# Kernel optimization log

Measured on AMD Instinct MI355X. Metric: run time of the kernel, lower is better.

Reference implementation:

```python
import jax, jax.numpy as jnp
import numpy as np

NT = 16          # nt_states
TS = 48          # t_states
T = NT + TS      # total states
B, N = 4, 24     # batch, sentence length
HUGE = 1.0e9


def setup_inputs():
    key = jax.random.key(0)
    k1, k2, k3 = jax.random.split(key, 3)
    unary_scores = jax.nn.log_softmax(jax.random.normal(k1, (B, N, T), jnp.float32), axis=-1)
    rule = jax.random.normal(k2, (B, NT, N, T, T, 2), jnp.float32)
    rule_scores = jax.nn.log_softmax(rule.reshape(B, NT, N, -1), axis=-1).reshape(B, NT, N, T, T, 2)
    root_scores = jax.nn.log_softmax(jax.random.normal(k3, (B, NT), jnp.float32), axis=-1)
    return {"unary_scores": unary_scores, "rule_scores": rule_scores, "root_scores": root_scores}


def _lse(x, axes):
    return jax.nn.logsumexp(x, axis=axes)


def _inside(unary_scores, rule_scores, root_scores):
    Bv, Nv, Tt = unary_scores.shape
    nt = rule_scores.shape[1]
    dt = unary_scores.dtype
    R = jnp.moveaxis(rule_scores, 5, 0)            # (D, B, Tparent, H, TL, TR)

    # beta[b,l,r,t,h]: headed inside chart; betau[b,l,r,t]: head-summed chart
    beta = jnp.full((Bv, Nv + 1, Nv + 1, Tt, Nv), -HUGE, dt)
    betau = jnp.full((Bv, Nv + 1, Nv + 1, Tt), -HUGE, dt)

    # width-1 spans: only terminal states (word_span_slice = nt:T, nt_emission=False)
    ks = np.arange(Nv)
    st = np.arange(nt, Tt)
    beta = beta.at[:, ks[:, None], ks[:, None] + 1, st[None, :], ks[:, None]].set(0.0)
    betau = betau.at[:, ks[:, None], ks[:, None] + 1, st[None, :]].set(
        unary_scores[:, ks[:, None], st[None, :]])

    nts = np.arange(nt)
    for W in range(2, Nv + 1):
        L = Nv - W + 1
        ls = np.arange(L)
        rs = ls + W
        hidx = ls[:, None] + np.arange(W)          # (L, W) absolute head positions

        def width_body(beta, betau, R, unary_scores, W=W, ls=ls, rs=rs, hidx=hidx):
            def chartH(la, ra, s0, s1):            # (B, L, S, W)
                x = beta[:, la, ra, s0:s1, :]
                return jnp.take_along_axis(x, hidx[None, :, None, :], axis=3)

            def chartU(la, ra, s0, s1):            # (B, L, S)
                return betau[:, la, ra, s0:s1]

            def rwin(d, a0, a1, c0, c1):           # (B, L, nt, W, A, C)
                r = R[d][:, :, hidx, a0:a1, c0:c1]
                return jnp.transpose(r, (0, 2, 1, 3, 4, 5))

            def comb(xH, yU, xU, yH, z0, z1):
                # D=0: head from left child; D=1: head from right child.
                # logsumexp over TL, TR and both directions -> (B, L, nt, W)
                left = (jnp.transpose(xH, (0, 1, 3, 2))[:, :, None, :, :, None]
                        + yU[:, :, None, None, None, :] + z0)
                right = (xU[:, :, None, None, :, None]
                         + jnp.transpose(yH, (0, 1, 3, 2))[:, :, None, :, None, :] + z1)
                return jnp.logaddexp(_lse(left, (-2, -1)), _lse(right, (-2, -1)))

            c0, c1 = (nt, Tt) if W == 2 else (0, nt)
            # split at l+1: left child is a single terminal
            tmp = comb(chartH(ls, ls + 1, nt, Tt), chartU(ls + 1, rs, c0, c1),
                       chartU(ls, ls + 1, nt, Tt), chartH(ls + 1, rs, c0, c1),
                       rwin(0, nt, Tt, c0, c1), rwin(1, nt, Tt, c0, c1))
            if W >= 3:
                # split at r-1: right child is a single terminal
                tmp = jnp.logaddexp(tmp, comb(
                    chartH(ls, rs - 1, 0, nt), chartU(rs - 1, rs, nt, Tt),
                    chartU(ls, rs - 1, 0, nt), chartH(rs - 1, rs, nt, Tt),
                    rwin(0, 0, nt, nt, Tt), rwin(1, 0, nt, nt, Tt)))
            if W >= 4:
                # interior splits: both children are nonterminal spans
                z0 = rwin(0, 0, nt, 0, nt)
                z1 = rwin(1, 0, nt, 0, nt)
                for wl in range(2, W - 1):
                    s = ls + wl
                    tmp = jnp.logaddexp(tmp, comb(
                        chartH(ls, s, 0, nt), chartU(s, rs, 0, nt),
                        chartU(ls, s, 0, nt), chartH(s, rs, 0, nt), z0, z1))
            # add head-word emission under the parent NT; sum heads for betau
            uw = jnp.transpose(unary_scores[:, hidx, :nt], (0, 1, 3, 2))  # (B,L,nt,W)
            return tmp, _lse(tmp + uw, -1)

        tmp, tmpu = jax.checkpoint(width_body)(beta, betau, R, unary_scores)
        beta = beta.at[:, ls[:, None, None], rs[:, None, None],
                       nts[None, :, None], hidx[:, None, :]].set(tmp)
        betau = betau.at[:, ls[:, None], rs[:, None], nts[None, :]].set(tmpu)

    return jax.nn.logsumexp(betau[:, 0, Nv, :nt] + root_scores, axis=-1)  # log Z, (B,)


_inside_jit = jax.jit(_inside)


def reference(unary_scores, rule_scores, root_scores):
    return _inside_jit(unary_scores, rule_scores, root_scores)
```

## Files before the change

kernel.cpp:

```cpp
#include <hip/hip_runtime.h>
#include <cstddef>

#define Bv 4
#define Nv 24
#define NTv 16
#define Tv 64
#define NP 25
#define NEGF (-1e30f)

#define BETAA_OFF 0
#define BETAU_OFF 960000
#define RNT_OFF   1120000
#define T0_OFF    1906432
#define T1_OFF    2496256
#define T0L_OFF   3086080
#define T1R_OFF   3110656
#define D0_OFF    3135232
#define D1_OFF    3136768
#define EU_OFF    3138304
#define PROG_OFF  3142912
#define WS_NEED   3143040

__device__ __forceinline__ void publish(float* p, float v) {
  *p = v;
  (void)__hip_atomic_exchange(p, v, __ATOMIC_RELAXED, __HIP_MEMORY_SCOPE_AGENT);
}

__global__ void init_kernel(const float* __restrict__ unary, float* __restrict__ betau,
                            float* __restrict__ Eu, int* __restrict__ prog) {
  int t = blockIdx.x * blockDim.x + threadIdx.x;
  if (t < Bv * 32) prog[t] = 0;
  if (t >= Bv * Nv * 48) return;
  int i = t % 48, kk = (t / 48) % Nv, b = t / (48 * Nv);
  float u = unary[(size_t)(b * Nv + kk) * Tv + 16 + i];
  betau[((size_t)(b * NP + kk) * NP + (kk + 1)) * Tv + 16 + i] = u;
  Eu[(size_t)(b * Nv + kk) * 48 + i] = __expf(u);
}

__global__ __launch_bounds__(256) void prep_kernel(
    const float* __restrict__ rule, const float* __restrict__ Eu,
    float* __restrict__ RNT, float* __restrict__ T0, float* __restrict__ T1,
    float* __restrict__ T0L, float* __restrict__ T1R,
    float* __restrict__ D0, float* __restrict__ D1) {
  const int h = blockIdx.x, A = blockIdx.y, b = blockIdx.z;
  const int t = threadIdx.x;
  __shared__ float er0[64 * 65];
  __shared__ float er1[64 * 65];
  __shared__ float E[24 * 48];
  __shared__ float red[256];

  for (int i = t; i < 24 * 48; i += 256) E[i] = Eu[(size_t)b * (24 * 48) + i];
  const float* rb = rule + (size_t)((b * NTv + A) * Nv + h) * 8192;
#pragma unroll
  for (int i = 0; i < 8; ++i) {
    int lin = i * 1024 + t * 4;
    float4 v = *(const float4*)(rb + lin);
    int sL = lin >> 7, rem = (lin & 127) >> 1;
    er0[sL * 65 + rem] = __expf(v.x);
    er1[sL * 65 + rem] = __expf(v.y);
    er0[sL * 65 + rem + 1] = __expf(v.z);
    er1[sL * 65 + rem + 1] = __expf(v.w);
  }
  __syncthreads();
  {
    float* dst0 = RNT + (((size_t)(b * 2 + 0) * Nv + h) * NTv + A) * 256;
    float* dst1 = RNT + (((size_t)(b * 2 + 1) * Nv + h) * NTv + A) * 256;
    dst0[t] = er0[(t >> 4) * 65 + (t & 15)];
    dst1[t] = er1[(t >> 4) * 65 + (t & 15)];
  }
  for (int o = t; o < 384; o += 256) {
    int p = o >> 4, sL = o & 15;
    const float* Ep = E + p * 48;
    const float* r0 = er0 + sL * 65 + 16;
    float acc = 0.f;
#pragma unroll 8
    for (int j = 0; j < 48; ++j) acc += Ep[j] * r0[j];
    T0[(((size_t)(b * Nv + h) * Nv + p) * NTv + sL) * NTv + A] = acc;
  }
  for (int o = t; o < 384; o += 256) {
    int p = o >> 4, sR = o & 15;
    const float* Ep = E + p * 48;
    float acc = 0.f;
#pragma unroll 8
    for (int i = 0; i < 48; ++i) acc += Ep[i] * er1[(16 + i) * 65 + sR];
    T1[(((size_t)(b * Nv + h) * Nv + p) * NTv + sR) * NTv + A] = acc;
  }
  if (t < 16) {
    float acc = 0.f;
    for (int i = 0; i < 48; ++i) acc += er0[(16 + i) * 65 + t];
    T0L[((size_t)(b * Nv + h) * NTv + t) * NTv + A] = acc;
  } else if (t < 32) {
    int sL = t - 16;
    float acc = 0.f;
    for (int j = 0; j < 48; ++j) acc += er1[sL * 65 + 16 + j];
    T1R[((size_t)(b * Nv + h) * NTv + sL) * NTv + A] = acc;
  }
  float acc0 = 0.f, acc1 = 0.f;
  const int hp = (h + 1 < 24) ? h + 1 : 0, hm = (h >= 1) ? h - 1 : 0;
  for (int e = t; e < 2304; e += 256) {
    int i = e / 48, j = e % 48;
    float r0 = er0[(16 + i) * 65 + 16 + j];
    float r1 = er1[(16 + i) * 65 + 16 + j];
    acc0 += E[hp * 48 + j] * r0;
    acc1 += E[hm * 48 + i] * r1;
  }
  red[t] = acc0;
  __syncthreads();
  if (t < 64) {
    float s = red[t] + red[t + 64] + red[t + 128] + red[t + 192];
#pragma unroll
    for (int off = 32; off; off >>= 1) s += __shfl_xor(s, off, 64);
    if (t == 0 && h <= 22) D0[((size_t)b * Nv + h) * NTv + A] = s;
  }
  __syncthreads();
  red[t] = acc1;
  __syncthreads();
  if (t < 64) {
    float s = red[t] + red[t + 64] + red[t + 128] + red[t + 192];
#pragma unroll
    for (int off = 32; off; off >>= 1) s += __shfl_xor(s, off, 64);
    if (t == 0 && h >= 1) D1[((size_t)b * Nv + (h - 1)) * NTv + A] = s;
  }
}

__device__ __forceinline__ float max16(float v) {
  v = fmaxf(v, __shfl_xor(v, 8, 16));
  v = fmaxf(v, __shfl_xor(v, 4, 16));
  v = fmaxf(v, __shfl_xor(v, 2, 16));
  v = fmaxf(v, __shfl_xor(v, 1, 16));
  return v;
}

__device__ __forceinline__ void edge_dot(float v0, float v1, float v2, float v3,
                                         const float* Tb, float& sh, float& S) {
  float mx = fmaxf(fmaxf(v0, v1), fmaxf(v2, v3));
  mx = fmaxf(mx, __shfl_xor(mx, 1, 64));
  mx = fmaxf(mx, __shfl_xor(mx, 2, 64));
  float dot = __expf(v0 - mx) * Tb[0] + __expf(v1 - mx) * Tb[16] +
              __expf(v2 - mx) * Tb[32] + __expf(v3 - mx) * Tb[48];
  dot += __shfl_xor(dot, 1, 64);
  dot += __shfl_xor(dot, 2, 64);
  sh = mx;
  S = dot;
}

#define MAXI 21

__global__ __launch_bounds__(768) void width_all_kernel(
    const float* __restrict__ unary, float* __restrict__ betaA, float* __restrict__ betau,
    const float* __restrict__ RNT, const float* __restrict__ T0, const float* __restrict__ T1,
    const float* __restrict__ T0L, const float* __restrict__ T1R,
    const float* __restrict__ D0, const float* __restrict__ D1,
    const float* __restrict__ root, float* __restrict__ out, int* __restrict__ colFlag) {
  const int rr = blockIdx.x, b = blockIdx.y;
  const int r = rr + 2;
  const int tid = threadIdx.x;
  int* flagb = colFlag + b * 32;

  __shared__ float chartC[23][384];
  __shared__ float buC[23][16];
  __shared__ float U0[24 * 256], U1[24 * 256];
  __shared__ float sG0[24], sG1[24];
  __shared__ float pM[2 * 24 * 16], pS[2 * 24 * 16];
  __shared__ float sTmp[16 * 24];

  for (int i = 0; i <= r - 2; ++i) {
    const int l = r - 2 - i;
    const int W = r - l;

    if (W >= 3) {
      if (tid < W - 2) {
        const int m = l + 2 + tid;
        while (__hip_atomic_load(&flagb[m], __ATOMIC_RELAXED,
                                 __HIP_MEMORY_SCOPE_AGENT) < m - l - 1)
          __builtin_amdgcn_s_sleep(1);
      }
      __syncthreads();
    }

    const int g = tid >> 5;
    const int k = tid & 31;
    float U0r[8], U1r[8];
#pragma unroll
    for (int j = 0; j < 8; ++j) { U0r[j] = 0.f; U1r[j] = 0.f; }
    float G0 = NEGF, G1 = NEGF;

    if (g < W) {
      const int hcol = l + g;
      float av1[MAXI], av0[MAXI];
      int e1 = min(l + g, r - 2);
      int cnt1 = e1 - (l + 2) + 1; if (cnt1 < 0) cnt1 = 0;
      if (k < 16) {
        const size_t base = ((size_t)(b * NP + l) * NP + (l + 2)) * Tv + k;
#pragma unroll
        for (int ii = 0; ii < MAXI; ++ii)
          if (ii < cnt1) av1[ii] = betau[base + (size_t)ii * Tv];
      } else {
#pragma unroll
        for (int ii = 0; ii < MAXI; ++ii)
          if (ii < cnt1) av1[ii] = chartC[l + 2 + ii][hcol * 16 + (k - 16)];
      }
      int m0 = max(l + g + 1, l + 2), e0 = r - 2;
      int cnt0 = e0 - m0 + 1; if (cnt0 < 0) cnt0 = 0;
      if (k < 16) {
        const size_t base = ((size_t)(b * NP + l) * NP + m0) * 384 + (size_t)hcol * 16 + k;
#pragma unroll
        for (int ii = 0; ii < MAXI; ++ii)
          if (ii < cnt0) av0[ii] = betaA[base + (size_t)ii * 384];
      } else {
#pragma unroll
        for (int ii = 0; ii < MAXI; ++ii)
          if (ii < cnt0) av0[ii] = buC[m0 + ii][k - 16];
      }
      float mx1 = NEGF, mx0 = NEGF;
#pragma unroll
      for (int ii = 0; ii < MAXI; ++ii) {
        if (ii < cnt1) mx1 = fmaxf(mx1, av1[ii]);
        if (ii < cnt0) mx0 = fmaxf(mx0, av0[ii]);
      }
      float o1 = max16(mx1), o0 = max16(mx0);
      float t1 = __shfl_xor(o1, 16, 32), t0 = __shfl_xor(o0, 16, 32);
      G1 = o1 + t1;
      G0 = o0 + t0;
#pragma unroll
      for (int ii = 0; ii < MAXI; ++ii) {
        if (ii < cnt1) {
          float e = __expf(av1[ii] - o1);
          float eR = __shfl(e, 16 + (k & 15), 32);
#pragma unroll
          for (int j = 0; j < 8; ++j)
            U1r[j] += __shfl(e, 2 * j + (k >> 4), 32) * eR;
        }
        if (ii < cnt0) {
          float e = __expf(av0[ii] - o0);
          float eR = __shfl(e, 16 + (k & 15), 32);
#pragma unroll
          for (int j = 0; j < 8; ++j)
            U0r[j] += __shfl(e, 2 * j + (k >> 4), 32) * eR;
        }
      }
#pragma unroll
      for (int j = 0; j < 8; ++j) {
        U0[g * 256 + k + 32 * j] = U0r[j];
        U1[g * 256 + k + 32 * j] = U1r[j];
      }
      if (k == 0) { sG0[g] = G0; sG1[g] = G1; }
    }
    __syncthreads();

    {
      const int w = tid >> 6, lane = tid & 63;
      const int A = lane >> 2, q = lane & 3;
      for (int p = w; p < 2 * W; p += 12) {
        const int hh = p >> 1, d = p & 1;
        const int h = l + hh;
        const float* Urow = (d ? U1 : U0) + hh * 256 + 4 * q;
        const float* Rb = RNT + (((size_t)(b * 2 + d) * Nv + h) * NTv + A) * 256 + 4 * q;
        float a0 = 0.f, a1 = 0.f, a2 = 0.f, a3 = 0.f;
#pragma unroll
        for (int sL = 0; sL < 16; ++sL) {
          float4 u = *(const float4*)(Urow + sL * 16);
          float4 rv = *(const float4*)(Rb + sL * 16);
          a0 += u.x * rv.x; a1 += u.y * rv.y; a2 += u.z * rv.z; a3 += u.w * rv.w;
        }
        float acc = (a0 + a1) + (a2 + a3);
        acc += __shfl_xor(acc, 1, 64);
        acc += __shfl_xor(acc, 2, 64);
        float Mi = d ? sG1[hh] : sG0[hh];
        float sh2 = NEGF, S2 = 0.f, sh3 = NEGF, S3 = 0.f;
        if (W >= 3) {
          if (d == 0) {
            if (hh < W - 1) {
              const float* Tb = T0 + (((size_t)(b * Nv + h) * Nv + (r - 1)) * NTv + 4 * q) * NTv + A;
              float4 e4 = *(const float4*)(betaA +
                  ((size_t)(b * NP + l) * NP + (r - 1)) * 384 + (size_t)h * 16 + 4 * q);
              edge_dot(e4.x, e4.y, e4.z, e4.w, Tb, sh2, S2);
            }
            if (hh == 0) {
              const float* Tb = T0L + ((size_t)(b * Nv + l) * NTv + 4 * q) * NTv + A;
              const float* u4 = &buC[l + 1][4 * q];
              edge_dot(u4[0], u4[1], u4[2], u4[3], Tb, sh3, S3);
            }
          } else {
            if (hh >= 1) {
              const float* Tb = T1 + (((size_t)(b * Nv + h) * Nv + l) * NTv + 4 * q) * NTv + A;
              const float* e4 = &chartC[l + 1][h * 16 + 4 * q];
              edge_dot(e4[0], e4[1], e4[2], e4[3], Tb, sh2, S2);
            }
            if (hh == W - 1) {
              const float* Tb = T1R + ((size_t)(b * Nv + (r - 1)) * NTv + 4 * q) * NTv + A;
              float4 u4 = *(const float4*)(betau +
                  ((size_t)(b * NP + l) * NP + (r - 1)) * Tv + 4 * q);
              edge_dot(u4.x, u4.y, u4.z, u4.w, Tb, sh3, S3);
            }
          }
        } else {
          if (d == 0 && hh == 0) { sh2 = 0.f; S2 = D0[((size_t)b * Nv + l) * NTv + A]; }
          if (d == 1 && hh == 1) { sh2 = 0.f; S2 = D1[((size_t)b * Nv + l) * NTv + A]; }
        }
        float Mf = fmaxf(Mi, fmaxf(sh2, sh3));
        float Sf = acc * __expf(Mi - Mf) + S2 * __expf(sh2 - Mf) + S3 * __expf(sh3 - Mf);
        if (q == 0) {
          pM[(d * 24 + hh) * 16 + A] = Mf;
          pS[(d * 24 + hh) * 16 + A] = Sf;
        }
      }
    }
    __syncthreads();

    if (tid < 384) {
      int A2 = tid & 15, hh = tid >> 4;
      if (hh < W) {
        float M0 = pM[(0 * 24 + hh) * 16 + A2], S0 = pS[(0 * 24 + hh) * 16 + A2];
        float M1 = pM[(1 * 24 + hh) * 16 + A2], S1 = pS[(1 * 24 + hh) * 16 + A2];
        float nm = fmaxf(M0, M1);
        float s = S0 * __expf(M0 - nm) + S1 * __expf(M1 - nm);
        float val = nm + __logf(s);
        publish(&betaA[((size_t)(b * NP + l) * NP + r) * 384 + (l + hh) * 16 + A2], val);
        chartC[l][(l + hh) * 16 + A2] = val;
        sTmp[A2 * 24 + hh] = val + unary[(size_t)(b * Nv + (l + hh)) * Tv + A2];
      }
    }
    __syncthreads();
    if (tid < 16) {
      float mx = NEGF;
      for (int x = 0; x < W; ++x) mx = fmaxf(mx, sTmp[tid * 24 + x]);
      float s = 0.f;
      for (int x = 0; x < W; ++x) s += __expf(sTmp[tid * 24 + x] - mx);
      float val = mx + __logf(s);
      publish(&betau[((size_t)(b * NP + l) * NP + r) * Tv + tid], val);
      buC[l][tid] = val;
    }
    if (tid == 0) {
      asm volatile("s_waitcnt vmcnt(0)" ::: "memory");
      (void)__hip_atomic_exchange(&flagb[r], i + 1, __ATOMIC_RELAXED,
                                  __HIP_MEMORY_SCOPE_AGENT);
    }
  }

  if (rr == 22) {
    __syncthreads();
    if (tid == 0) {
      float vals[NTv];
      float mx = NEGF;
#pragma unroll
      for (int A = 0; A < NTv; ++A) {
        float v = buC[0][A] + root[b * NTv + A];
        vals[A] = v;
        mx = fmaxf(mx, v);
      }
      float s = 0.f;
#pragma unroll
      for (int A = 0; A < NTv; ++A) s += __expf(vals[A] - mx);
      out[b] = mx + __logf(s);
    }
  }
}

__global__ __launch_bounds__(768) void width_kernel_fb(
    const float* __restrict__ unary, const float* __restrict__ rule,
    float* __restrict__ betaA, float* __restrict__ betau, int W) {
  const int l = blockIdx.x, b = blockIdx.y;
  const int r = l + W;
  const int tid = threadIdx.x;
  const int sub = tid & 1;
  const int pid = tid >> 1;
  const int A = pid & 15;
  const int hh = pid >> 4;
  const int h = l + hh;
  const bool act = (hh < W);
  const int sA = tid & 15, sH = tid >> 4;

  __shared__ float sER0[48], sEL1[48];
  __shared__ float sCL0[16 * 24], sCR1[16 * 24];
  __shared__ float sMaxL0[24], sMaxR1[24];
  __shared__ float sShR0, sShL1;
  __shared__ float sTmp[16 * 24];

  float runM = NEGF, runS = 0.f;
  for (int m = l + 1; m < r; ++m) {
    const int wl = m - l, wr = r - m;
    if (tid < 64) {
      const int n = (wr == 1) ? 48 : 16, s0 = (wr == 1) ? 16 : 0;
      float v = (tid < n) ? betau[(size_t)((b * NP + m) * NP + r) * Tv + s0 + tid] : NEGF;
      float mx = v;
#pragma unroll
      for (int off = 32; off; off >>= 1) mx = fmaxf(mx, __shfl_xor(mx, off, 64));
      if (tid == 0) sShR0 = mx;
      if (tid < n) sER0[tid] = v - mx;
    } else if (tid < 128) {
      const int j = tid - 64;
      const int n = (wl == 1) ? 48 : 16, s0 = (wl == 1) ? 16 : 0;
      float v = (j < n) ? betau[(size_t)((b * NP + l) * NP + m) * Tv + s0 + j] : NEGF;
      float mx = v;
#pragma unroll
      for (int off = 32; off; off >>= 1) mx = fmaxf(mx, __shfl_xor(mx, off, 64));
      if (j == 0) sShL1 = mx;
      if (j < n) sEL1[j] = v - mx;
    }
    if (tid < 384) {
      if (wl > 1 && sH < wl) {
        float v = betaA[(size_t)((b * NP + l) * NP + m) * 384 + sA * Nv + (l + sH)];
        float mx = v;
#pragma unroll
        for (int off = 8; off; off >>= 1) mx = fmaxf(mx, __shfl_xor(mx, off, 16));
        if (sA == 0) sMaxL0[sH] = mx;
        sCL0[sA * Nv + sH] = v - mx;
      }
      if (wr > 1 && sH >= wl && sH < W) {
        float v = betaA[(size_t)((b * NP + m) * NP + r) * 384 + sA * Nv + (l + sH)];
        float mx = v;
#pragma unroll
        for (int off = 8; off; off >>= 1) mx = fmaxf(mx, __shfl_xor(mx, off, 16));
        if (sA == 0) sMaxR1[sH] = mx;
        sCR1[sA * Nv + sH] = v - mx;
      }
    }
    __syncthreads();
    if (act) {
      if (hh < wl && (wl > 1 || hh == 0)) {
        const int nL = (wl == 1) ? 48 : 16, sL0 = (wl == 1) ? 16 : 0;
        const int nR = (wr == 1) ? 48 : 16, sR0 = (wr == 1) ? 16 : 0;
        const float shift = ((wl == 1) ? 0.f : sMaxL0[hh]) + sShR0;
        float part = 0.f;
        const float* rb = rule + (size_t)(((b * NTv + A) * Nv + h) * Tv) * Tv * 2;
        for (int i = sub; i < nL; i += 2) {
          const float cl = (wl == 1) ? 0.f : sCL0[i * Nv + hh];
          const float* rp = rb + (size_t)(sL0 + i) * Tv * 2 + sR0 * 2;
#pragma unroll 8
          for (int j = 0; j < nR; ++j) part += __expf(cl + sER0[j] + rp[j * 2]);
        }
        float nm = fmaxf(runM, shift);
        runS = runS * __expf(runM - nm) + part * __expf(shift - nm);
        runM = nm;
      }
      if (hh >= wl && (wr > 1 || hh == W - 1)) {
        const int nL = (wl == 1) ? 48 : 16, sL0 = (wl == 1) ? 16 : 0;
        const int nR = (wr == 1) ? 48 : 16, sR0 = (wr == 1) ? 16 : 0;
        const float shift = sShL1 + ((wr == 1) ? 0.f : sMaxR1[hh]);
        float part = 0.f;
        const float* rb = rule + (size_t)(((b * NTv + A) * Nv + h) * Tv) * Tv * 2 + 1;
        for (int i = sub; i < nL; i += 2) {
          const float el = sEL1[i];
          const float* rp = rb + (size_t)(sL0 + i) * Tv * 2 + sR0 * 2;
#pragma unroll 8
          for (int j = 0; j < nR; ++j) {
            const float cr = (wr == 1) ? 0.f : sCR1[j * Nv + hh];
            part += __expf(el + cr + rp[j * 2]);
          }
        }
        float nm = fmaxf(runM, shift);
        runS = runS * __expf(runM - nm) + part * __expf(shift - nm);
        runM = nm;
      }
    }
    __syncthreads();
  }
  if (act) {
    float om = __shfl_xor(runM, 1, 64);
    float os = __shfl_xor(runS, 1, 64);
    float nm = fmaxf(runM, om);
    float s = runS * __expf(runM - nm) + os * __expf(om - nm);
    if (sub == 0) {
      float val = nm + __logf(s);
      betaA[(size_t)((b * NP + l) * NP + r) * 384 + A * Nv + h] = val;
      sTmp[A * Nv + hh] = val + unary[(b * Nv + h) * Tv + A];
    }
  }
  __syncthreads();
  if (tid < 16) {
    float mx = NEGF;
    for (int x = 0; x < W; ++x) mx = fmaxf(mx, sTmp[tid * Nv + x]);
    float s = 0.f;
    for (int x = 0; x < W; ++x) s += __expf(sTmp[tid * Nv + x] - mx);
    betau[(size_t)((b * NP + l) * NP + r) * Tv + tid] = mx + __logf(s);
  }
}

__global__ void final_kernel(const float* __restrict__ betau, const float* __restrict__ root,
                             float* __restrict__ out) {
  int b = threadIdx.x;
  if (b < Bv) {
    float vals[NTv];
    float mx = NEGF;
#pragma unroll
    for (int A = 0; A < NTv; ++A) {
      float v = betau[(size_t)((b * NP + 0) * NP + Nv) * Tv + A] + root[b * NTv + A];
      vals[A] = v;
      mx = fmaxf(mx, v);
    }
    float s = 0.f;
#pragma unroll
    for (int A = 0; A < NTv; ++A) s += __expf(vals[A] - mx);
    out[b] = mx + __logf(s);
  }
}

extern "C" void kernel_launch(void* const* d_in, const int* in_sizes, int n_in,
                              void* d_out, int out_size, void* d_ws, size_t ws_size,
                              hipStream_t stream) {
  (void)in_sizes; (void)n_in; (void)out_size;
  const float* unary = (const float*)d_in[0];
  const float* rule  = (const float*)d_in[1];
  const float* root  = (const float*)d_in[2];
  float* out = (float*)d_out;
  float* ws = (float*)d_ws;
  float* betaA = ws + BETAA_OFF;
  float* betau = ws + BETAU_OFF;
  const bool fast = ws_size >= (size_t)WS_NEED * sizeof(float);

  if (fast) {
    float* RNT = ws + RNT_OFF;
    float* T0  = ws + T0_OFF;
    float* T1  = ws + T1_OFF;
    float* T0L = ws + T0L_OFF;
    float* T1R = ws + T1R_OFF;
    float* D0  = ws + D0_OFF;
    float* D1  = ws + D1_OFF;
    float* Eu  = ws + EU_OFF;
    int* colFlag = (int*)(ws + PROG_OFF);
    init_kernel<<<(Bv * Nv * 48 + 255) / 256, 256, 0, stream>>>(unary, betau, Eu, colFlag);
    prep_kernel<<<dim3(24, 16, 4), 256, 0, stream>>>(rule, Eu, RNT, T0, T1, T0L, T1R, D0, D1);
    void* args[] = {(void*)&unary, (void*)&betaA, (void*)&betau, (void*)&RNT,
                    (void*)&T0, (void*)&T1, (void*)&T0L, (void*)&T1R,
                    (void*)&D0, (void*)&D1, (void*)&root, (void*)&out, (void*)&colFlag};
    hipLaunchCooperativeKernel((const void*)width_all_kernel, dim3(Nv - 1, Bv), dim3(768),
                               args, 0, stream);
  } else {
    float* Eu = ws + BETAU_OFF + 160000;
    int* prog = (int*)(ws + BETAU_OFF + 160000 + 4608);
    init_kernel<<<(Bv * Nv * 48 + 255) / 256, 256, 0, stream>>>(unary, betau, Eu, prog);
    for (int W = 2; W <= Nv; ++W) {
      dim3 grid(Nv - W + 1, Bv);
      width_kernel_fb<<<grid, 768, 0, stream>>>(unary, rule, betaA, betau, W);
    }
    final_kernel<<<1, 64, 0, stream>>>(betau, root, out);
  }
}
```

Before: 491.1 us.

## Split each chart column across multiple blocks with per-cell dependency flags

Each right-endpoint column of the CKY chart was processed serially by a single block. It is now split across `split` blocks (2 or 4, chosen from the reported occupancy), which take interleaved left endpoints. The per-column progress counters become per-cell ready flags, and each cell waits on exactly the cells it depends on. Because a column's cells are no longer all computed by one block, the shared-memory column caches are dropped and those values are read from global memory. The aim is more parallelism along the serial dependency chain, at the cost of more global loads and finer-grained spin-waiting.

Measured after the change: 901.1 us. 1.83x slower.

```diff
diff --git a/kernel.cpp b/kernel.cpp
--- a/kernel.cpp
+++ b/kernel.cpp
@@ -18,8 +18,8 @@
 #define D0_OFF    3135232
 #define D1_OFF    3136768
 #define EU_OFF    3138304
-#define PROG_OFF  3142912
-#define WS_NEED   3143040
+#define CELLF_OFF 3142912
+#define WS_NEED   3145412
 
 __device__ __forceinline__ void publish(float* p, float v) {
   *p = v;
@@ -27,9 +27,9 @@
 }
 
 __global__ void init_kernel(const float* __restrict__ unary, float* __restrict__ betau,
-                            float* __restrict__ Eu, int* __restrict__ prog) {
+                            float* __restrict__ Eu, int* __restrict__ cellF) {
   int t = blockIdx.x * blockDim.x + threadIdx.x;
-  if (t < Bv * 32) prog[t] = 0;
+  if (t < Bv * NP * NP) cellF[t] = 0;
   if (t >= Bv * Nv * 48) return;
   int i = t % 48, kk = (t / 48) % Nv, b = t / (48 * Nv);
   float u = unary[(size_t)(b * Nv + kk) * Tv + 16 + i];
@@ -146,33 +146,40 @@
 
 #define MAXI 21
 
-__global__ __launch_bounds__(768) void width_all_kernel(
+__global__ __launch_bounds__(768, 6) void width_all_kernel(
     const float* __restrict__ unary, float* __restrict__ betaA, float* __restrict__ betau,
     const float* __restrict__ RNT, const float* __restrict__ T0, const float* __restrict__ T1,
     const float* __restrict__ T0L, const float* __restrict__ T1R,
     const float* __restrict__ D0, const float* __restrict__ D1,
-    const float* __restrict__ root, float* __restrict__ out, int* __restrict__ colFlag) {
-  const int rr = blockIdx.x, b = blockIdx.y;
+    const float* __restrict__ root, float* __restrict__ out,
+    int* __restrict__ cellF, int split) {
+  const int rr = blockIdx.x, sidx = blockIdx.y, b = blockIdx.z;
   const int r = rr + 2;
   const int tid = threadIdx.x;
-  int* flagb = colFlag + b * 32;
-
-  __shared__ float chartC[23][384];
-  __shared__ float buC[23][16];
+  int* flagb = cellF + b * (NP * NP);
+
   __shared__ float U0[24 * 256], U1[24 * 256];
   __shared__ float sG0[24], sG1[24];
   __shared__ float pM[2 * 24 * 16], pS[2 * 24 * 16];
   __shared__ float sTmp[16 * 24];
-
-  for (int i = 0; i <= r - 2; ++i) {
+  __shared__ float sFin[16];
+
+  for (int i = sidx; i <= r - 2; i += split) {
     const int l = r - 2 - i;
     const int W = r - l;
 
     if (W >= 3) {
-      if (tid < W - 2) {
-        const int m = l + 2 + tid;
-        while (__hip_atomic_load(&flagb[m], __ATOMIC_RELAXED,
-                                 __HIP_MEMORY_SCOPE_AGENT) < m - l - 1)
+      const int nd = 2 * W - 4;
+      if (tid < nd) {
+        int li, ri;
+        if (tid == 0)      { li = l;     ri = r - 1; }
+        else if (tid == 1) { li = l + 1; ri = r;     }
+        else {
+          int j = (tid - 2) >> 1, m = l + 2 + j;
+          if ((tid & 1) == 0) { li = l; ri = m; } else { li = m; ri = r; }
+        }
+        while (__hip_atomic_load(&flagb[li * NP + ri], __ATOMIC_RELAXED,
+                                 __HIP_MEMORY_SCOPE_AGENT) == 0)
           __builtin_amdgcn_s_sleep(1);
       }
       __syncthreads();
@@ -196,9 +203,11 @@
         for (int ii = 0; ii < MAXI; ++ii)
           if (ii < cnt1) av1[ii] = betau[base + (size_t)ii * Tv];
       } else {
+        const size_t base = (size_t)(b * NP) * NP * 384 + (size_t)r * 384 +
+                            (size_t)hcol * 16 + (k - 16);
 #pragma unroll
         for (int ii = 0; ii < MAXI; ++ii)
-          if (ii < cnt1) av1[ii] = chartC[l + 2 + ii][hcol * 16 + (k - 16)];
+          if (ii < cnt1) av1[ii] = betaA[base + (size_t)(l + 2 + ii) * (NP * 384)];
       }
       int m0 = max(l + g + 1, l + 2), e0 = r - 2;
       int cnt0 = e0 - m0 + 1; if (cnt0 < 0) cnt0 = 0;
@@ -208,9 +217,10 @@
         for (int ii = 0; ii < MAXI; ++ii)
           if (ii < cnt0) av0[ii] = betaA[base + (size_t)ii * 384];
       } else {
+        const size_t base = (size_t)(b * NP) * NP * Tv + (size_t)r * Tv + (k - 16);
 #pragma unroll
         for (int ii = 0; ii < MAXI; ++ii)
-          if (ii < cnt0) av0[ii] = buC[m0 + ii][k - 16];
+          if (ii < cnt0) av0[ii] = betau[base + (size_t)(m0 + ii) * (NP * Tv)];
       }
       float mx1 = NEGF, mx0 = NEGF;
 #pragma unroll
@@ -278,14 +288,16 @@
             }
             if (hh == 0) {
               const float* Tb = T0L + ((size_t)(b * Nv + l) * NTv + 4 * q) * NTv + A;
-              const float* u4 = &buC[l + 1][4 * q];
-              edge_dot(u4[0], u4[1], u4[2], u4[3], Tb, sh3, S3);
+              float4 u4 = *(const float4*)(betau +
+                  ((size_t)(b * NP + (l + 1)) * NP + r) * Tv + 4 * q);
+              edge_dot(u4.x, u4.y, u4.z, u4.w, Tb, sh3, S3);
             }
           } else {
             if (hh >= 1) {
               const float* Tb = T1 + (((size_t)(b * Nv + h) * Nv + l) * NTv + 4 * q) * NTv + A;
-              const float* e4 = &chartC[l + 1][h * 16 + 4 * q];
-              edge_dot(e4[0], e4[1], e4[2], e4[3], Tb, sh2, S2);
+              float4 e4 = *(const float4*)(betaA +
+                  ((size_t)(b * NP + (l + 1)) * NP + r) * 384 + (size_t)h * 16 + 4 * q);
+              edge_dot(e4.x, e4.y, e4.z, e4.w, Tb, sh2, S2);
             }
             if (hh == W - 1) {
               const float* Tb = T1R + ((size_t)(b * Nv + (r - 1)) * NTv + 4 * q) * NTv + A;
@@ -317,7 +329,6 @@
         float s = S0 * __expf(M0 - nm) + S1 * __expf(M1 - nm);
         float val = nm + __logf(s);
         publish(&betaA[((size_t)(b * NP + l) * NP + r) * 384 + (l + hh) * 16 + A2], val);
-        chartC[l][(l + hh) * 16 + A2] = val;
         sTmp[A2 * 24 + hh] = val + unary[(size_t)(b * Nv + (l + hh)) * Tv + A2];
       }
     }
@@ -329,23 +340,23 @@
       for (int x = 0; x < W; ++x) s += __expf(sTmp[tid * 24 + x] - mx);
       float val = mx + __logf(s);
       publish(&betau[((size_t)(b * NP + l) * NP + r) * Tv + tid], val);
-      buC[l][tid] = val;
+      if (l == 0 && r == Nv) sFin[tid] = val;
     }
     if (tid == 0) {
       asm volatile("s_waitcnt vmcnt(0)" ::: "memory");
-      (void)__hip_atomic_exchange(&flagb[r], i + 1, __ATOMIC_RELAXED,
+      (void)__hip_atomic_exchange(&flagb[l * NP + r], 1, __ATOMIC_RELAXED,
                                   __HIP_MEMORY_SCOPE_AGENT);
     }
   }
 
-  if (rr == 22) {
+  if (rr == Nv - 2 && sidx == ((Nv - 2) % split)) {
     __syncthreads();
     if (tid == 0) {
       float vals[NTv];
       float mx = NEGF;
 #pragma unroll
       for (int A = 0; A < NTv; ++A) {
-        float v = buC[0][A] + root[b * NTv + A];
+        float v = sFin[A] + root[b * NTv + A];
         vals[A] = v;
         mx = fmaxf(mx, v);
       }
@@ -518,14 +529,18 @@
     float* D0  = ws + D0_OFF;
     float* D1  = ws + D1_OFF;
     float* Eu  = ws + EU_OFF;
-    int* colFlag = (int*)(ws + PROG_OFF);
-    init_kernel<<<(Bv * Nv * 48 + 255) / 256, 256, 0, stream>>>(unary, betau, Eu, colFlag);
+    int* cellF = (int*)(ws + CELLF_OFF);
+    init_kernel<<<(Bv * Nv * 48 + 255) / 256, 256, 0, stream>>>(unary, betau, Eu, cellF);
     prep_kernel<<<dim3(24, 16, 4), 256, 0, stream>>>(rule, Eu, RNT, T0, T1, T0L, T1R, D0, D1);
+    int occ = 0;
+    (void)hipOccupancyMaxActiveBlocksPerMultiprocessor(&occ, width_all_kernel, 768, 0);
+    int split = (occ >= 2) ? 4 : 2;
     void* args[] = {(void*)&unary, (void*)&betaA, (void*)&betau, (void*)&RNT,
                     (void*)&T0, (void*)&T1, (void*)&T0L, (void*)&T1R,
-                    (void*)&D0, (void*)&D1, (void*)&root, (void*)&out, (void*)&colFlag};
-    hipLaunchCooperativeKernel((const void*)width_all_kernel, dim3(Nv - 1, Bv), dim3(768),
-                               args, 0, stream);
+                    (void*)&D0, (void*)&D1, (void*)&root, (void*)&out,
+                    (void*)&cellF, (void*)&split};
+    hipLaunchCooperativeKernel((const void*)width_all_kernel, dim3(Nv - 1, split, Bv),
+                               dim3(768), args, 0, stream);
   } else {
     float* Eu = ws + BETAU_OFF + 160000;
     int* prog = (int*)(ws + BETAU_OFF + 160000 + 4608);
```

## Use per-cell readiness flags, bf16 rule table, and plain atomic stores

Applied to the files above, without the earlier changes.

Replaces the per-column progress counters with per-cell ready flags. The wait on the immediately preceding cell (l, r-1) is deferred until just before the edge term that reads it, so the U accumulation can overlap with that dependency. Also stores the exponentiated nonterminal rule table as packed bf16 pairs to halve its load traffic in the hot dot product, and replaces the store-plus-exchange publish with a single atomic store. The bf16 rounding lowers precision of the rule probabilities, and the finer-grained flags add more polling locations.

Result: faster. 464.6 us (-5.4%).

```diff
diff --git a/kernel.cpp b/kernel.cpp
--- a/kernel.cpp
+++ b/kernel.cpp
@@ -18,18 +18,24 @@
 #define D0_OFF    3135232
 #define D1_OFF    3136768
 #define EU_OFF    3138304
-#define PROG_OFF  3142912
-#define WS_NEED   3143040
+#define CELLF_OFF 3142912
+#define WS_NEED   3145412
 
 __device__ __forceinline__ void publish(float* p, float v) {
-  *p = v;
-  (void)__hip_atomic_exchange(p, v, __ATOMIC_RELAXED, __HIP_MEMORY_SCOPE_AGENT);
+  __hip_atomic_store(p, v, __ATOMIC_RELAXED, __HIP_MEMORY_SCOPE_AGENT);
+}
+
+__device__ __forceinline__ unsigned packbf2(float lo, float hi) {
+  unsigned bl = __float_as_uint(lo), bh = __float_as_uint(hi);
+  bl = (bl + 0x7FFFu + ((bl >> 16) & 1u)) >> 16;
+  bh = (bh + 0x7FFFu + ((bh >> 16) & 1u)) >> 16;
+  return (bh << 16) | bl;
 }
 
 __global__ void init_kernel(const float* __restrict__ unary, float* __restrict__ betau,
-                            float* __restrict__ Eu, int* __restrict__ prog) {
+                            float* __restrict__ Eu, int* __restrict__ cellF) {
   int t = blockIdx.x * blockDim.x + threadIdx.x;
-  if (t < Bv * 32) prog[t] = 0;
+  if (t < Bv * NP * NP) cellF[t] = 0;
   if (t >= Bv * Nv * 48) return;
   int i = t % 48, kk = (t / 48) % Nv, b = t / (48 * Nv);
   float u = unary[(size_t)(b * Nv + kk) * Tv + 16 + i];
@@ -39,7 +45,7 @@
 
 __global__ __launch_bounds__(256) void prep_kernel(
     const float* __restrict__ rule, const float* __restrict__ Eu,
-    float* __restrict__ RNT, float* __restrict__ T0, float* __restrict__ T1,
+    unsigned* __restrict__ RNTh, float* __restrict__ T0, float* __restrict__ T1,
     float* __restrict__ T0L, float* __restrict__ T1R,
     float* __restrict__ D0, float* __restrict__ D1) {
   const int h = blockIdx.x, A = blockIdx.y, b = blockIdx.z;
@@ -63,10 +69,16 @@
   }
   __syncthreads();
   {
-    float* dst0 = RNT + (((size_t)(b * 2 + 0) * Nv + h) * NTv + A) * 256;
-    float* dst1 = RNT + (((size_t)(b * 2 + 1) * Nv + h) * NTv + A) * 256;
-    dst0[t] = er0[(t >> 4) * 65 + (t & 15)];
-    dst1[t] = er1[(t >> 4) * 65 + (t & 15)];
+    unsigned* dst0 = RNTh + (((size_t)(b * 2 + 0) * Nv + h) * NTv + A) * 128;
+    unsigned* dst1 = RNTh + (((size_t)(b * 2 + 1) * Nv + h) * NTv + A) * 128;
+    if (t < 128) {
+      int sL = t >> 3, sRp = t & 7;
+      dst0[t] = packbf2(er0[sL * 65 + 2 * sRp], er0[sL * 65 + 2 * sRp + 1]);
+    } else {
+      int t2 = t - 128;
+      int sL = t2 >> 3, sRp = t2 & 7;
+      dst1[t2] = packbf2(er1[sL * 65 + 2 * sRp], er1[sL * 65 + 2 * sRp + 1]);
+    }
   }
   for (int o = t; o < 384; o += 256) {
     int p = o >> 4, sL = o & 15;
@@ -148,14 +160,14 @@
 
 __global__ __launch_bounds__(768) void width_all_kernel(
     const float* __restrict__ unary, float* __restrict__ betaA, float* __restrict__ betau,
-    const float* __restrict__ RNT, const float* __restrict__ T0, const float* __restrict__ T1,
+    const unsigned* __restrict__ RNTh, const float* __restrict__ T0, const float* __restrict__ T1,
     const float* __restrict__ T0L, const float* __restrict__ T1R,
     const float* __restrict__ D0, const float* __restrict__ D1,
-    const float* __restrict__ root, float* __restrict__ out, int* __restrict__ colFlag) {
+    const float* __restrict__ root, float* __restrict__ out, int* __restrict__ cellF) {
   const int rr = blockIdx.x, b = blockIdx.y;
   const int r = rr + 2;
   const int tid = threadIdx.x;
-  int* flagb = colFlag + b * 32;
+  int* flagb = cellF + b * (NP * NP);
 
   __shared__ float chartC[23][384];
   __shared__ float buC[23][16];
@@ -168,11 +180,11 @@
     const int l = r - 2 - i;
     const int W = r - l;
 
-    if (W >= 3) {
-      if (tid < W - 2) {
+    if (W >= 4) {
+      if (tid < W - 3) {
         const int m = l + 2 + tid;
-        while (__hip_atomic_load(&flagb[m], __ATOMIC_RELAXED,
-                                 __HIP_MEMORY_SCOPE_AGENT) < m - l - 1)
+        while (__hip_atomic_load(&flagb[l * NP + m], __ATOMIC_RELAXED,
+                                 __HIP_MEMORY_SCOPE_AGENT) == 0)
           __builtin_amdgcn_s_sleep(1);
       }
       __syncthreads();
@@ -249,19 +261,28 @@
     __syncthreads();
 
     {
+      if (W >= 3) {
+        while (__hip_atomic_load(&flagb[l * NP + (r - 1)], __ATOMIC_RELAXED,
+                                 __HIP_MEMORY_SCOPE_AGENT) == 0)
+          __builtin_amdgcn_s_sleep(1);
+      }
       const int w = tid >> 6, lane = tid & 63;
       const int A = lane >> 2, q = lane & 3;
       for (int p = w; p < 2 * W; p += 12) {
         const int hh = p >> 1, d = p & 1;
         const int h = l + hh;
         const float* Urow = (d ? U1 : U0) + hh * 256 + 4 * q;
-        const float* Rb = RNT + (((size_t)(b * 2 + d) * Nv + h) * NTv + A) * 256 + 4 * q;
+        const unsigned* Rb = RNTh + (((size_t)(b * 2 + d) * Nv + h) * NTv + A) * 128 + 2 * q;
         float a0 = 0.f, a1 = 0.f, a2 = 0.f, a3 = 0.f;
 #pragma unroll
         for (int sL = 0; sL < 16; ++sL) {
           float4 u = *(const float4*)(Urow + sL * 16);
-          float4 rv = *(const float4*)(Rb + sL * 16);
-          a0 += u.x * rv.x; a1 += u.y * rv.y; a2 += u.z * rv.z; a3 += u.w * rv.w;
+          uint2 rv = *(const uint2*)(Rb + sL * 8);
+          float r0 = __uint_as_float(rv.x << 16);
+          float r1 = __uint_as_float(rv.x & 0xFFFF0000u);
+          float r2 = __uint_as_float(rv.y << 16);
+          float r3 = __uint_as_float(rv.y & 0xFFFF0000u);
+          a0 += u.x * r0; a1 += u.y * r1; a2 += u.z * r2; a3 += u.w * r3;
         }
         float acc = (a0 + a1) + (a2 + a3);
         acc += __shfl_xor(acc, 1, 64);
@@ -333,8 +354,8 @@
     }
     if (tid == 0) {
       asm volatile("s_waitcnt vmcnt(0)" ::: "memory");
-      (void)__hip_atomic_exchange(&flagb[r], i + 1, __ATOMIC_RELAXED,
-                                  __HIP_MEMORY_SCOPE_AGENT);
+      __hip_atomic_store(&flagb[l * NP + r], 1, __ATOMIC_RELAXED,
+                         __HIP_MEMORY_SCOPE_AGENT);
     }
   }
 
@@ -510,7 +531,7 @@
   const bool fast = ws_size >= (size_t)WS_NEED * sizeof(float);
 
   if (fast) {
-    float* RNT = ws + RNT_OFF;
+    unsigned* RNTh = (unsigned*)(ws + RNT_OFF);
     float* T0  = ws + T0_OFF;
     float* T1  = ws + T1_OFF;
     float* T0L = ws + T0L_OFF;
@@ -518,12 +539,12 @@
     float* D0  = ws + D0_OFF;
     float* D1  = ws + D1_OFF;
     float* Eu  = ws + EU_OFF;
-    int* colFlag = (int*)(ws + PROG_OFF);
-    init_kernel<<<(Bv * Nv * 48 + 255) / 256, 256, 0, stream>>>(unary, betau, Eu, colFlag);
-    prep_kernel<<<dim3(24, 16, 4), 256, 0, stream>>>(rule, Eu, RNT, T0, T1, T0L, T1R, D0, D1);
-    void* args[] = {(void*)&unary, (void*)&betaA, (void*)&betau, (void*)&RNT,
+    int* cellF = (int*)(ws + CELLF_OFF);
+    init_kernel<<<(Bv * Nv * 48 + 255) / 256, 256, 0, stream>>>(unary, betau, Eu, cellF);
+    prep_kernel<<<dim3(24, 16, 4), 256, 0, stream>>>(rule, Eu, RNTh, T0, T1, T0L, T1R, D0, D1);
+    void* args[] = {(void*)&unary, (void*)&betaA, (void*)&betau, (void*)&RNTh,
                     (void*)&T0, (void*)&T1, (void*)&T0L, (void*)&T1R,
-                    (void*)&D0, (void*)&D1, (void*)&root, (void*)&out, (void*)&colFlag};
+                    (void*)&D0, (void*)&D1, (void*)&root, (void*)&out, (void*)&cellF};
     hipLaunchCooperativeKernel((const void*)width_all_kernel, dim3(Nv - 1, Bv), dim3(768),
                                args, 0, stream);
   } else {
```
